# Performance work log

Hardware: AMD Instinct MI355X
Metric: run time of the kernel (lower is better)

The kernel has to match this reference:

```python
import jax, jax.numpy as jnp
import numpy as np

SPARSITY = 0.9   # config.pruning_parameters.sparsity (self.r)
TEMP = 0.01      # config.pruning_parameters.temperature
D_MODEL, D_FF = 4096, 16384


def setup_inputs() -> dict:
    key = jax.random.key(0)
    weight = jax.random.normal(key, (D_MODEL, D_FF), dtype=jnp.float32)
    return {"weight": weight}


def reference(weight):
    # PDP.get_mask (unstructured path) followed by mask * weight.
    n = weight.size  # static
    # Full descending sort of |weight|, exactly as ops.top_k(abs_flat, size)
    w_all = jax.lax.top_k(jnp.abs(weight).ravel(), n)[0]
    # ind = cast((1 - r) * N, int32) - 1, clipped to [0, N-2]; static since shapes are static
    ind = int((1.0 - SPARSITY) * n) - 1
    lim = min(max(ind, 0), n - 2)
    Wh = w_all[lim]
    Wt = w_all[lim + 1]
    t = 0.5 * (Wh + Wt)  # threshold order statistic
    # softmax over the pair (t^2, w^2)/temp, keep second component:
    # mw = exp(w^2/T) / (exp(t^2/T) + exp(w^2/T)) = sigmoid((w^2 - t^2)/T)
    mw = jax.nn.sigmoid((weight * weight - t * t) / TEMP)
    return mw * weight
```

## Files before the change

kernel.cpp:

```cpp
#include <hip/hip_runtime.h>


#define NBC  4096
#define NBSF 12288
#define NBF2 2048

typedef float    v4f __attribute__((ext_vector_type(4)));
typedef unsigned v4u __attribute__((ext_vector_type(4)));

__global__ void zero_ws(unsigned* __restrict__ ws, int n) {
    int i = blockIdx.x * blockDim.x + threadIdx.x;
    if (i < n) ws[i] = 0;
}

__global__ void sample_hist(const v4u* __restrict__ in, unsigned* __restrict__ gh) {
    __shared__ unsigned h[NBC];
    for (int i = threadIdx.x; i < NBC; i += blockDim.x) h[i] = 0;
    __syncthreads();
    const v4u* p = in + (size_t)blockIdx.x * 16384;
    #pragma unroll
    for (int k = 0; k < 4; ++k) {
        v4u v = p[threadIdx.x + k * 256];
        atomicAdd(&h[(v.x & 0x7fffffffu) >> 19], 1u);
        atomicAdd(&h[(v.y & 0x7fffffffu) >> 19], 1u);
        atomicAdd(&h[(v.z & 0x7fffffffu) >> 19], 1u);
        atomicAdd(&h[(v.w & 0x7fffffffu) >> 19], 1u);
    }
    __syncthreads();
    for (int i = threadIdx.x; i < NBC; i += blockDim.x) {
        unsigned c = h[i];
        if (c) atomicAdd(&gh[i], c);
    }
}

__global__ void scan_sample(const unsigned* __restrict__ gh, unsigned* __restrict__ res,
                            unsigned sample_need) {
    __shared__ unsigned bins[NBC];
    __shared__ unsigned part[256];
    __shared__ unsigned sup[16];
    unsigned s = 0;
    for (int j = 0; j < 16; ++j) {
        int idx = threadIdx.x * 16 + j;
        unsigned c = gh[NBC - 1 - idx];
        bins[idx] = c;
        s += c;
    }
    part[threadIdx.x] = s;
    __syncthreads();
    if (threadIdx.x < 16) {
        unsigned t = 0;
        for (int j = 0; j < 16; ++j) t += part[threadIdx.x * 16 + j];
        sup[threadIdx.x] = t;
    }
    __syncthreads();
    if (threadIdx.x == 0) {
        unsigned accum = 0; int sb = 15;
        for (int i = 0; i < 16; ++i) { unsigned nx = accum + sup[i]; if (nx >= sample_need) { sb = i; break; } accum = nx; }
        int pb = sb * 16 + 15;
        for (int i = sb * 16; i < sb * 16 + 16; ++i) { unsigned nx = accum + part[i]; if (nx >= sample_need) { pb = i; break; } accum = nx; }
        int d = pb * 16 + 15;
        for (int i = pb * 16; i < pb * 16 + 16; ++i) { unsigned nx = accum + bins[i]; if (nx >= sample_need) { d = i; break; } accum = nx; }
        unsigned b_est = (unsigned)(NBC - 1 - d);
        res[0] = (b_est > 0) ? b_est - 1u : 0u;
        res[1] = (b_est < NBC - 1) ? b_est + 1u : (unsigned)(NBC - 1);
    }
}

__global__ void sample_fine_hist(const v4u* __restrict__ in, unsigned* __restrict__ res,
                                 unsigned* __restrict__ gh) {
    __shared__ unsigned h[NBSF];
    __shared__ unsigned red[256];
    const unsigned lo = res[0] << 19;
    const unsigned hi = (res[1] + 1u) << 19;
    for (int i = threadIdx.x; i < NBSF; i += blockDim.x) h[i] = 0;
    __syncthreads();
    unsigned above = 0;
    const v4u* p = in + (size_t)blockIdx.x * 16384;
    #pragma unroll
    for (int k = 0; k < 4; ++k) {
        v4u v = p[threadIdx.x + k * 256];
        #pragma unroll
        for (int j = 0; j < 4; ++j) {
            unsigned u = v[j] & 0x7fffffffu;
            if (u >= hi) ++above;
            else if (u >= lo) atomicAdd(&h[(u - lo) >> 7], 1u);
        }
    }
    red[threadIdx.x] = above;
    __syncthreads();
    for (int s = 128; s > 0; s >>= 1) {
        if (threadIdx.x < (unsigned)s) red[threadIdx.x] += red[threadIdx.x + s];
        __syncthreads();
    }
    if (threadIdx.x == 0 && red[0]) atomicAdd(&res[4], red[0]);
    for (int i = threadIdx.x; i < NBSF; i += blockDim.x) {
        unsigned c = h[i];
        if (c) atomicAdd(&gh[i], c);
    }
}

__global__ void scan_sample2(const unsigned* __restrict__ gh, unsigned* __restrict__ res,
                             unsigned sample_need) {
    __shared__ unsigned bins[NBSF];
    __shared__ unsigned part[256];
    __shared__ unsigned sup[16];
    unsigned s = 0;
    for (int j = 0; j < 48; ++j) {
        int idx = threadIdx.x * 48 + j;
        unsigned c = gh[NBSF - 1 - idx];
        bins[idx] = c;
        s += c;
    }
    part[threadIdx.x] = s;
    __syncthreads();
    if (threadIdx.x < 16) {
        unsigned t = 0;
        for (int j = 0; j < 16; ++j) t += part[threadIdx.x * 16 + j];
        sup[threadIdx.x] = t;
    }
    __syncthreads();
    if (threadIdx.x == 0) {
        unsigned accum = res[4];
        int sb = 15;
        for (int i = 0; i < 16; ++i) { unsigned nx = accum + sup[i]; if (nx >= sample_need) { sb = i; break; } accum = nx; }
        int pb = sb * 16 + 15;
        for (int i = sb * 16; i < sb * 16 + 16; ++i) { unsigned nx = accum + part[i]; if (nx >= sample_need) { pb = i; break; } accum = nx; }
        int d = pb * 48 + 47;
        for (int i = pb * 48; i < pb * 48 + 48; ++i) { unsigned nx = accum + bins[i]; if (nx >= sample_need) { d = i; break; } accum = nx; }
        int kc = NBSF - 1 - d;
        int kb = kc - (NBF2 / 2);
        if (kb < 0) kb = 0;
        if (kb > NBSF - NBF2) kb = NBSF - NBF2;
        res[5] = (unsigned)kb;
    }
}

__global__ void fine_hist(const v4u* __restrict__ in, unsigned* __restrict__ res,
                          unsigned* __restrict__ gh, int n4) {
    __shared__ unsigned h[NBF2];
    __shared__ unsigned red[256];
    const unsigned lo2 = (res[0] << 19) + (res[5] << 7);
    const unsigned hi2 = lo2 + ((unsigned)NBF2 << 7);
    for (int i = threadIdx.x; i < NBF2; i += blockDim.x) h[i] = 0;
    __syncthreads();
    unsigned above = 0;
    const int stride = gridDim.x * blockDim.x;
    int i = blockIdx.x * blockDim.x + threadIdx.x;
    for (; i + stride < n4; i += 2 * stride) {
        v4u a = in[i];
        v4u b = in[i + stride];
        #pragma unroll
        for (int k = 0; k < 4; ++k) {
            unsigned u = a[k] & 0x7fffffffu;
            if (u >= hi2) ++above;
            else if (u >= lo2) atomicAdd(&h[(u - lo2) >> 7], 1u);
        }
        #pragma unroll
        for (int k = 0; k < 4; ++k) {
            unsigned u = b[k] & 0x7fffffffu;
            if (u >= hi2) ++above;
            else if (u >= lo2) atomicAdd(&h[(u - lo2) >> 7], 1u);
        }
    }
    if (i < n4) {
        v4u a = in[i];
        #pragma unroll
        for (int k = 0; k < 4; ++k) {
            unsigned u = a[k] & 0x7fffffffu;
            if (u >= hi2) ++above;
            else if (u >= lo2) atomicAdd(&h[(u - lo2) >> 7], 1u);
        }
    }
    red[threadIdx.x] = above;
    __syncthreads();
    for (int s = 128; s > 0; s >>= 1) {
        if (threadIdx.x < (unsigned)s) red[threadIdx.x] += red[threadIdx.x + s];
        __syncthreads();
    }
    if (threadIdx.x == 0 && red[0]) atomicAdd(&res[2], red[0]);
    for (int i2 = threadIdx.x; i2 < NBF2; i2 += blockDim.x) {
        unsigned c = h[i2];
        if (c) atomicAdd(&gh[i2], c);
    }
}

__global__ void scan_fine(const unsigned* __restrict__ gh, unsigned* __restrict__ res,
                          unsigned need_h, unsigned need_t) {
    __shared__ unsigned bins[NBF2];
    __shared__ unsigned part[256];
    __shared__ unsigned sup[16];
    unsigned s = 0;
    #pragma unroll
    for (int j = 0; j < 8; ++j) {
        int idx = threadIdx.x * 8 + j;
        unsigned c = gh[NBF2 - 1 - idx];
        bins[idx] = c;
        s += c;
    }
    part[threadIdx.x] = s;
    __syncthreads();
    if (threadIdx.x < 16) {
        unsigned t = 0;
        for (int j = 0; j < 16; ++j) t += part[threadIdx.x * 16 + j];
        sup[threadIdx.x] = t;
    }
    __syncthreads();
    if (threadIdx.x == 0) {
        const unsigned lo2 = (res[0] << 19) + (res[5] << 7);
        const unsigned base = res[2];
        unsigned needs[2] = { need_h, need_t };
        unsigned keys[2];
        for (int q = 0; q < 2; ++q) {
            unsigned accum = base; int sb = 15;
            for (int i = 0; i < 16; ++i) { unsigned nx = accum + sup[i]; if (nx >= needs[q]) { sb = i; break; } accum = nx; }
            int pb = sb * 16 + 15;
            for (int i = sb * 16; i < sb * 16 + 16; ++i) { unsigned nx = accum + part[i]; if (nx >= needs[q]) { pb = i; break; } accum = nx; }
            int d = pb * 8 + 7;
            for (int i = pb * 8; i < pb * 8 + 8; ++i) { unsigned nx = accum + bins[i]; if (nx >= needs[q]) { d = i; break; } accum = nx; }
            keys[q] = (unsigned)(NBF2 - 1 - d);
        }
        float Wh = __uint_as_float(lo2 + (keys[0] << 7) + 64u);
        float Wt = __uint_as_float(lo2 + (keys[1] << 7) + 64u);
        float t  = 0.5f * (Wh + Wt);
        res[3] = __float_as_uint(t * t);
    }
}

__global__ void apply_mask(const v4f* __restrict__ in, v4f* __restrict__ out,
                           const unsigned* __restrict__ res, int n4) {
    float t2 = __uint_as_float(res[3]);
    int stride = gridDim.x * blockDim.x;
    for (int i = blockIdx.x * blockDim.x + threadIdx.x; i < n4; i += stride) {
        v4f w = in[i];
        v4f o;
        o.x = w.x * __builtin_amdgcn_rcpf(1.0f + __expf((t2 - w.x * w.x) * 100.0f));
        o.y = w.y * __builtin_amdgcn_rcpf(1.0f + __expf((t2 - w.y * w.y) * 100.0f));
        o.z = w.z * __builtin_amdgcn_rcpf(1.0f + __expf((t2 - w.z * w.z) * 100.0f));
        o.w = w.w * __builtin_amdgcn_rcpf(1.0f + __expf((t2 - w.w * w.w) * 100.0f));
        __builtin_nontemporal_store(o, &out[i]);
    }
}

extern "C" void kernel_launch(void* const* d_in, const int* in_sizes, int n_in,
                              void* d_out, int out_size, void* d_ws, size_t ws_size,
                              hipStream_t stream) {
    const int n = in_sizes[0];
    const int n4 = n / 4;
    const v4u* in4 = (const v4u*)d_in[0];

    unsigned* ws      = (unsigned*)d_ws;
    unsigned* hist_s  = ws;
    unsigned* hist_sf = ws + NBC;
    unsigned* hist_f  = ws + NBC + NBSF;
    unsigned* res     = ws + NBC + NBSF + NBF2;

    int ind = (int)((1.0 - 0.9) * (double)n) - 1;
    int lim = ind < 0 ? 0 : ind;
    if (lim > n - 2) lim = n - 2;
    unsigned need_h = (unsigned)lim + 1u;
    unsigned need_t = (unsigned)lim + 2u;

    const unsigned SAMPLE = 1024u * 4096u;
    unsigned sample_need = (unsigned)((double)need_h * (double)SAMPLE / (double)n);
    if (sample_need == 0) sample_need = 1;

    const int nz = NBC + NBSF + NBF2 + 8;
    zero_ws<<<(nz + 255) / 256, 256, 0, stream>>>(ws, nz);
    sample_hist<<<1024, 256, 0, stream>>>(in4, hist_s);
    scan_sample<<<1, 256, 0, stream>>>(hist_s, res, sample_need);
    sample_fine_hist<<<1024, 256, 0, stream>>>(in4, res, hist_sf);
    scan_sample2<<<1, 256, 0, stream>>>(hist_sf, res, sample_need);
    fine_hist<<<4096, 256, 0, stream>>>(in4, res, hist_f, n4);
    scan_fine<<<1, 256, 0, stream>>>(hist_f, res, need_h, need_t);
    apply_mask<<<8192, 256, 0, stream>>>((const v4f*)d_in[0], (v4f*)d_out, res, n4);
}
```

Before: 544.7 us.

## Fuse histogram scans into last-block epilogues and replace zero kernel with memset

Each single-block scan kernel is folded into its histogram kernel: the last block to finish, detected through an atomic completion counter, performs the scan. The zeroing kernel becomes a hipMemsetAsync, and the sigmoid uses exp2f with a prescaled constant. This removes three kernel launches and their serialization gaps, at the cost of a threadfence and a global atomic per block. It also relies on correct atomic-load visibility of the merged histograms.

```diff
diff --git a/kernel.cpp b/kernel.cpp
--- a/kernel.cpp
+++ b/kernel.cpp
@@ -8,14 +8,18 @@
 typedef float    v4f __attribute__((ext_vector_type(4)));
 typedef unsigned v4u __attribute__((ext_vector_type(4)));
 
-__global__ void zero_ws(unsigned* __restrict__ ws, int n) {
-    int i = blockIdx.x * blockDim.x + threadIdx.x;
-    if (i < n) ws[i] = 0;
-}
-
-__global__ void sample_hist(const v4u* __restrict__ in, unsigned* __restrict__ gh) {
+__device__ __forceinline__ unsigned gload(const unsigned* p) {
+    return __hip_atomic_load(p, __ATOMIC_RELAXED, __HIP_MEMORY_SCOPE_AGENT);
+}
+
+__global__ void sample_hist_scan(const v4u* __restrict__ in, unsigned* __restrict__ gh,
+                                 unsigned* __restrict__ res, unsigned* __restrict__ done,
+                                 unsigned sample_need) {
     __shared__ unsigned h[NBC];
-    for (int i = threadIdx.x; i < NBC; i += blockDim.x) h[i] = 0;
+    __shared__ unsigned part[256];
+    __shared__ unsigned sup[16];
+    __shared__ unsigned lastflag;
+    for (int i = threadIdx.x; i < NBC; i += 256) h[i] = 0;
     __syncthreads();
     const v4u* p = in + (size_t)blockIdx.x * 16384;
     #pragma unroll
@@ -27,22 +31,24 @@
         atomicAdd(&h[(v.w & 0x7fffffffu) >> 19], 1u);
     }
     __syncthreads();
-    for (int i = threadIdx.x; i < NBC; i += blockDim.x) {
+    for (int i = threadIdx.x; i < NBC; i += 256) {
         unsigned c = h[i];
         if (c) atomicAdd(&gh[i], c);
     }
-}
-
-__global__ void scan_sample(const unsigned* __restrict__ gh, unsigned* __restrict__ res,
-                            unsigned sample_need) {
-    __shared__ unsigned bins[NBC];
-    __shared__ unsigned part[256];
-    __shared__ unsigned sup[16];
+    __syncthreads();
+    if (threadIdx.x == 0) {
+        __threadfence();
+        unsigned t = atomicAdd(&done[0], 1u);
+        lastflag = (t == gridDim.x - 1u) ? 1u : 0u;
+    }
+    __syncthreads();
+    if (!lastflag) return;
+    __threadfence();
     unsigned s = 0;
     for (int j = 0; j < 16; ++j) {
         int idx = threadIdx.x * 16 + j;
-        unsigned c = gh[NBC - 1 - idx];
-        bins[idx] = c;
+        unsigned c = gload(&gh[NBC - 1 - idx]);
+        h[idx] = c;
         s += c;
     }
     part[threadIdx.x] = s;
@@ -59,20 +65,23 @@
         int pb = sb * 16 + 15;
         for (int i = sb * 16; i < sb * 16 + 16; ++i) { unsigned nx = accum + part[i]; if (nx >= sample_need) { pb = i; break; } accum = nx; }
         int d = pb * 16 + 15;
-        for (int i = pb * 16; i < pb * 16 + 16; ++i) { unsigned nx = accum + bins[i]; if (nx >= sample_need) { d = i; break; } accum = nx; }
+        for (int i = pb * 16; i < pb * 16 + 16; ++i) { unsigned nx = accum + h[i]; if (nx >= sample_need) { d = i; break; } accum = nx; }
         unsigned b_est = (unsigned)(NBC - 1 - d);
         res[0] = (b_est > 0) ? b_est - 1u : 0u;
         res[1] = (b_est < NBC - 1) ? b_est + 1u : (unsigned)(NBC - 1);
     }
 }
 
-__global__ void sample_fine_hist(const v4u* __restrict__ in, unsigned* __restrict__ res,
-                                 unsigned* __restrict__ gh) {
+__global__ void sample_fine_scan(const v4u* __restrict__ in, unsigned* __restrict__ gh,
+                                 unsigned* __restrict__ res, unsigned* __restrict__ done,
+                                 unsigned sample_need) {
     __shared__ unsigned h[NBSF];
-    __shared__ unsigned red[256];
+    __shared__ unsigned part[256];
+    __shared__ unsigned sup[16];
+    __shared__ unsigned lastflag;
     const unsigned lo = res[0] << 19;
     const unsigned hi = (res[1] + 1u) << 19;
-    for (int i = threadIdx.x; i < NBSF; i += blockDim.x) h[i] = 0;
+    for (int i = threadIdx.x; i < NBSF; i += 256) h[i] = 0;
     __syncthreads();
     unsigned above = 0;
     const v4u* p = in + (size_t)blockIdx.x * 16384;
@@ -86,29 +95,31 @@
             else if (u >= lo) atomicAdd(&h[(u - lo) >> 7], 1u);
         }
     }
-    red[threadIdx.x] = above;
+    part[threadIdx.x] = above;
     __syncthreads();
     for (int s = 128; s > 0; s >>= 1) {
-        if (threadIdx.x < (unsigned)s) red[threadIdx.x] += red[threadIdx.x + s];
+        if (threadIdx.x < (unsigned)s) part[threadIdx.x] += part[threadIdx.x + s];
         __syncthreads();
     }
-    if (threadIdx.x == 0 && red[0]) atomicAdd(&res[4], red[0]);
-    for (int i = threadIdx.x; i < NBSF; i += blockDim.x) {
+    if (threadIdx.x == 0 && part[0]) atomicAdd(&res[4], part[0]);
+    for (int i = threadIdx.x; i < NBSF; i += 256) {
         unsigned c = h[i];
         if (c) atomicAdd(&gh[i], c);
     }
-}
-
-__global__ void scan_sample2(const unsigned* __restrict__ gh, unsigned* __restrict__ res,
-                             unsigned sample_need) {
-    __shared__ unsigned bins[NBSF];
-    __shared__ unsigned part[256];
-    __shared__ unsigned sup[16];
+    __syncthreads();
+    if (threadIdx.x == 0) {
+        __threadfence();
+        unsigned t = atomicAdd(&done[1], 1u);
+        lastflag = (t == gridDim.x - 1u) ? 1u : 0u;
+    }
+    __syncthreads();
+    if (!lastflag) return;
+    __threadfence();
     unsigned s = 0;
     for (int j = 0; j < 48; ++j) {
         int idx = threadIdx.x * 48 + j;
-        unsigned c = gh[NBSF - 1 - idx];
-        bins[idx] = c;
+        unsigned c = gload(&gh[NBSF - 1 - idx]);
+        h[idx] = c;
         s += c;
     }
     part[threadIdx.x] = s;
@@ -120,13 +131,13 @@
     }
     __syncthreads();
     if (threadIdx.x == 0) {
-        unsigned accum = res[4];
+        unsigned accum = gload(&res[4]);
         int sb = 15;
         for (int i = 0; i < 16; ++i) { unsigned nx = accum + sup[i]; if (nx >= sample_need) { sb = i; break; } accum = nx; }
         int pb = sb * 16 + 15;
         for (int i = sb * 16; i < sb * 16 + 16; ++i) { unsigned nx = accum + part[i]; if (nx >= sample_need) { pb = i; break; } accum = nx; }
         int d = pb * 48 + 47;
-        for (int i = pb * 48; i < pb * 48 + 48; ++i) { unsigned nx = accum + bins[i]; if (nx >= sample_need) { d = i; break; } accum = nx; }
+        for (int i = pb * 48; i < pb * 48 + 48; ++i) { unsigned nx = accum + h[i]; if (nx >= sample_need) { d = i; break; } accum = nx; }
         int kc = NBSF - 1 - d;
         int kb = kc - (NBF2 / 2);
         if (kb < 0) kb = 0;
@@ -135,13 +146,16 @@
     }
 }
 
-__global__ void fine_hist(const v4u* __restrict__ in, unsigned* __restrict__ res,
-                          unsigned* __restrict__ gh, int n4) {
+__global__ void fine_hist_scan(const v4u* __restrict__ in, unsigned* __restrict__ gh,
+                               unsigned* __restrict__ res, unsigned* __restrict__ done,
+                               int n4, unsigned need_h, unsigned need_t) {
     __shared__ unsigned h[NBF2];
-    __shared__ unsigned red[256];
+    __shared__ unsigned part[256];
+    __shared__ unsigned sup[16];
+    __shared__ unsigned lastflag;
     const unsigned lo2 = (res[0] << 19) + (res[5] << 7);
     const unsigned hi2 = lo2 + ((unsigned)NBF2 << 7);
-    for (int i = threadIdx.x; i < NBF2; i += blockDim.x) h[i] = 0;
+    for (int i = threadIdx.x; i < NBF2; i += 256) h[i] = 0;
     __syncthreads();
     unsigned above = 0;
     const int stride = gridDim.x * blockDim.x;
@@ -171,30 +185,32 @@
             else if (u >= lo2) atomicAdd(&h[(u - lo2) >> 7], 1u);
         }
     }
-    red[threadIdx.x] = above;
+    part[threadIdx.x] = above;
     __syncthreads();
     for (int s = 128; s > 0; s >>= 1) {
-        if (threadIdx.x < (unsigned)s) red[threadIdx.x] += red[threadIdx.x + s];
+        if (threadIdx.x < (unsigned)s) part[threadIdx.x] += part[threadIdx.x + s];
         __syncthreads();
     }
-    if (threadIdx.x == 0 && red[0]) atomicAdd(&res[2], red[0]);
-    for (int i2 = threadIdx.x; i2 < NBF2; i2 += blockDim.x) {
+    if (threadIdx.x == 0 && part[0]) atomicAdd(&res[2], part[0]);
+    for (int i2 = threadIdx.x; i2 < NBF2; i2 += 256) {
         unsigned c = h[i2];
         if (c) atomicAdd(&gh[i2], c);
     }
-}
-
-__global__ void scan_fine(const unsigned* __restrict__ gh, unsigned* __restrict__ res,
-                          unsigned need_h, unsigned need_t) {
-    __shared__ unsigned bins[NBF2];
-    __shared__ unsigned part[256];
-    __shared__ unsigned sup[16];
+    __syncthreads();
+    if (threadIdx.x == 0) {
+        __threadfence();
+        unsigned t = atomicAdd(&done[2], 1u);
+        lastflag = (t == gridDim.x - 1u) ? 1u : 0u;
+    }
+    __syncthreads();
+    if (!lastflag) return;
+    __threadfence();
     unsigned s = 0;
     #pragma unroll
     for (int j = 0; j < 8; ++j) {
         int idx = threadIdx.x * 8 + j;
-        unsigned c = gh[NBF2 - 1 - idx];
-        bins[idx] = c;
+        unsigned c = gload(&gh[NBF2 - 1 - idx]);
+        h[idx] = c;
         s += c;
     }
     part[threadIdx.x] = s;
@@ -206,17 +222,16 @@
     }
     __syncthreads();
     if (threadIdx.x == 0) {
-        const unsigned lo2 = (res[0] << 19) + (res[5] << 7);
-        const unsigned base = res[2];
+        const unsigned base = gload(&res[2]);
         unsigned needs[2] = { need_h, need_t };
         unsigned keys[2];
         for (int q = 0; q < 2; ++q) {
             unsigned accum = base; int sb = 15;
-            for (int i = 0; i < 16; ++i) { unsigned nx = accum + sup[i]; if (nx >= needs[q]) { sb = i; break; } accum = nx; }
+            for (int i2 = 0; i2 < 16; ++i2) { unsigned nx = accum + sup[i2]; if (nx >= needs[q]) { sb = i2; break; } accum = nx; }
             int pb = sb * 16 + 15;
-            for (int i = sb * 16; i < sb * 16 + 16; ++i) { unsigned nx = accum + part[i]; if (nx >= needs[q]) { pb = i; break; } accum = nx; }
+            for (int i2 = sb * 16; i2 < sb * 16 + 16; ++i2) { unsigned nx = accum + part[i2]; if (nx >= needs[q]) { pb = i2; break; } accum = nx; }
             int d = pb * 8 + 7;
-            for (int i = pb * 8; i < pb * 8 + 8; ++i) { unsigned nx = accum + bins[i]; if (nx >= needs[q]) { d = i; break; } accum = nx; }
+            for (int i2 = pb * 8; i2 < pb * 8 + 8; ++i2) { unsigned nx = accum + h[i2]; if (nx >= needs[q]) { d = i2; break; } accum = nx; }
             keys[q] = (unsigned)(NBF2 - 1 - d);
         }
         float Wh = __uint_as_float(lo2 + (keys[0] << 7) + 64u);
@@ -230,13 +245,14 @@
                            const unsigned* __restrict__ res, int n4) {
     float t2 = __uint_as_float(res[3]);
     int stride = gridDim.x * blockDim.x;
+    const float C = 144.269504089f;
     for (int i = blockIdx.x * blockDim.x + threadIdx.x; i < n4; i += stride) {
         v4f w = in[i];
         v4f o;
-        o.x = w.x * __builtin_amdgcn_rcpf(1.0f + __expf((t2 - w.x * w.x) * 100.0f));
-        o.y = w.y * __builtin_amdgcn_rcpf(1.0f + __expf((t2 - w.y * w.y) * 100.0f));
-        o.z = w.z * __builtin_amdgcn_rcpf(1.0f + __expf((t2 - w.z * w.z) * 100.0f));
-        o.w = w.w * __builtin_amdgcn_rcpf(1.0f + __expf((t2 - w.w * w.w) * 100.0f));
+        o.x = w.x * __builtin_amdgcn_rcpf(1.0f + exp2f((t2 - w.x * w.x) * C));
+        o.y = w.y * __builtin_amdgcn_rcpf(1.0f + exp2f((t2 - w.y * w.y) * C));
+        o.z = w.z * __builtin_amdgcn_rcpf(1.0f + exp2f((t2 - w.z * w.z) * C));
+        o.w = w.w * __builtin_amdgcn_rcpf(1.0f + exp2f((t2 - w.w * w.w) * C));
         __builtin_nontemporal_store(o, &out[i]);
     }
 }
@@ -253,6 +269,7 @@
     unsigned* hist_sf = ws + NBC;
     unsigned* hist_f  = ws + NBC + NBSF;
     unsigned* res     = ws + NBC + NBSF + NBF2;
+    unsigned* done    = res + 8;
 
     int ind = (int)((1.0 - 0.9) * (double)n) - 1;
     int lim = ind < 0 ? 0 : ind;
@@ -264,13 +281,10 @@
     unsigned sample_need = (unsigned)((double)need_h * (double)SAMPLE / (double)n);
     if (sample_need == 0) sample_need = 1;
 
-    const int nz = NBC + NBSF + NBF2 + 8;
-    zero_ws<<<(nz + 255) / 256, 256, 0, stream>>>(ws, nz);
-    sample_hist<<<1024, 256, 0, stream>>>(in4, hist_s);
-    scan_sample<<<1, 256, 0, stream>>>(hist_s, res, sample_need);
-    sample_fine_hist<<<1024, 256, 0, stream>>>(in4, res, hist_sf);
-    scan_sample2<<<1, 256, 0, stream>>>(hist_sf, res, sample_need);
-    fine_hist<<<4096, 256, 0, stream>>>(in4, res, hist_f, n4);
-    scan_fine<<<1, 256, 0, stream>>>(hist_f, res, need_h, need_t);
+    const size_t nz = (size_t)(NBC + NBSF + NBF2 + 8 + 4) * sizeof(unsigned);
+    hipMemsetAsync(ws, 0, nz, stream);
+    sample_hist_scan<<<1024, 256, 0, stream>>>(in4, hist_s, res, done, sample_need);
+    sample_fine_scan<<<1024, 256, 0, stream>>>(in4, hist_sf, res, done, sample_need);
+    fine_hist_scan<<<4096, 256, 0, stream>>>(in4, hist_f, res, done, n4, need_h, need_t);
     apply_mask<<<8192, 256, 0, stream>>>((const v4f*)d_in[0], (v4f*)d_out, res, n4);
 }
```

New measurement: 745.2 us. 1.37x slower.
